# Performance work log

Hardware: AMD Instinct MI355X
Metric: run time of the kernel (lower is better)

## Reference

```python
import jax, jax.numpy as jnp
import numpy as np
from itertools import product

B = 2
X, Y, Z = 96, 96, 192          # voxel grid (x, y, t)
NPB = 300_000                   # occupied voxels per batch item
PX, PY, PZ = X // 2, Y // 2, Z // 4  # pooled grid (kernel/stride [2,2,4])
CIN, COUT, KVOL, NCONV = 32, 64, 27, 2
EPS = 1e-5


def _build_maps():
    """Builds sparse coordinates, maxpool segment ids and 3x3x3 conv kernel maps
    (gather/scatter index pairs per kernel offset), mirroring MinkowskiEngine's
    coordinate manager."""
    rng = np.random.default_rng(0)
    coords = []
    for b in range(B):
        lin = rng.choice(X * Y * Z, NPB, replace=False)
        x = lin // (Y * Z)
        y = (lin // Z) % Y
        z = lin % Z
        coords.append(np.stack([np.full(NPB, b), x, y, z], 1))
    c = np.concatenate(coords).astype(np.int64)  # [N,4] (b,x,y,z)
    # max-pool coord map: out coord = (x//2, y//2, z//4)
    pk = ((c[:, 0] * PX + c[:, 1] // 2) * PY + c[:, 2] // 2) * PZ + c[:, 3] // 4
    uniq, inv = np.unique(pk, return_inverse=True)
    M = len(uniq)
    pz = uniq % PZ
    py = (uniq // PZ) % PY
    px = (uniq // (PZ * PY)) % PX
    pb = uniq // (PZ * PY * PX)
    lut = np.full(B * PX * PY * PZ, -1, np.int64)
    lut[uniq] = np.arange(M)
    ins, outs = [], []
    for dx, dy, dz in product((-1, 0, 1), repeat=3):
        nx, ny, nz = px + dx, py + dy, pz + dz
        ok = (nx >= 0) & (nx < PX) & (ny >= 0) & (ny < PY) & (nz >= 0) & (nz < PZ)
        nk = ((pb * PX + np.clip(nx, 0, PX - 1)) * PY + np.clip(ny, 0, PY - 1)) * PZ + np.clip(nz, 0, PZ - 1)
        j = np.where(ok, lut[nk], -1)
        sel = j >= 0
        ins.append(j[sel])
        outs.append(np.arange(M)[sel])
    L = max(len(a) for a in ins)
    ci = np.full((KVOL, L), M, np.int64)  # pad -> index M (zero row)
    co = np.full((KVOL, L), M, np.int64)  # pad -> dummy out row M (dropped)
    for k in range(KVOL):
        ci[k, : len(ins[k])] = ins[k]
        co[k, : len(outs[k])] = outs[k]
    return inv.astype(np.int64), ci, co, M


def setup_inputs() -> dict:
    key = jax.random.key(0)
    ks = jax.random.split(key, 4)
    pool_seg, ci, co, M = _build_maps()
    N = B * NPB
    feats = jax.random.normal(ks[0], (N, CIN), jnp.float32)
    Wd = jax.random.normal(ks[1], (CIN, COUT), jnp.float32) / np.sqrt(CIN)
    W1 = jax.random.normal(ks[2], (KVOL, COUT, COUT), jnp.float32) / np.sqrt(KVOL * COUT)
    W2 = jax.random.normal(ks[3], (KVOL, COUT, COUT), jnp.float32) / np.sqrt(KVOL * COUT)
    ones = jnp.ones((COUT,), jnp.float32)
    zeros = jnp.zeros((COUT,), jnp.float32)
    return {
        "feats": feats, "Wd": Wd,
        "g0": ones, "b0": zeros,
        "W1": W1, "g1": ones, "b1": zeros,
        "W2": W2, "g2": ones, "b2": zeros,
        "pool_seg": jnp.asarray(pool_seg),
        "conv_in": jnp.asarray(ci), "conv_out": jnp.asarray(co),
        "num_pooled": int(M),
    }


def _bn(h, g, b):
    # training-mode batch norm over all sparse points (biased variance, eps=1e-5)
    m = h.mean(0)
    v = jnp.mean((h - m) ** 2, 0)
    return (h - m) * (g / jnp.sqrt(v + EPS)) + b


def _sparse_conv(h, W, conv_in, conv_out, M):
    # gather-GEMM-scatter over 27 kernel offsets (MinkowskiConvolution, bias=False)
    C = W.shape[-1]
    hp = jnp.concatenate([h, jnp.zeros((1, h.shape[1]), h.dtype)])  # zero pad row
    out = jnp.zeros((M + 1, C), h.dtype)
    for k in range(W.shape[0]):
        out = out.at[conv_out[k]].add(hp[conv_in[k]] @ W[k])
    return out[:M]


def reference(feats, Wd, g0, b0, W1, g1, b1, W2, g2, b2,
              pool_seg, conv_in, conv_out, num_pooled):
    # down_conv (1x1, bias=False) -> BN -> ELU
    h = jax.nn.elu(_bn(feats @ Wd, g0, b0))
    # MinkowskiMaxPooling kernel=stride=[2,2,4] == segment max over pooled cells
    down = jax.ops.segment_max(h, pool_seg, num_segments=num_pooled)
    # nConvs LUConv blocks: ELU(BN(conv3x3x3(x)))
    o = down
    for W, g, b in ((W1, g1, b1), (W2, g2, b2)):
        o = jax.nn.elu(_bn(_sparse_conv(o, W, conv_in, conv_out, num_pooled), g, b))
    # residual add + ELU
    return jax.nn.elu(o + down)
```

## Files before the change

kernel.cpp:

```cpp
#include <hip/hip_runtime.h>
#include <math.h>

#define CIN  32
#define COUT 64
#define KVOL 27
#define EPSF 1e-5f

typedef __attribute__((ext_vector_type(8))) short          short8;
typedef __attribute__((ext_vector_type(8))) unsigned short u16x8;
typedef __attribute__((ext_vector_type(4))) float          float4v;

__device__ __forceinline__ float eluf(float x) { return x > 0.f ? x : expm1f(x); }

__device__ __forceinline__ unsigned short f2bf(float x) {
    unsigned u = __float_as_uint(x);
    unsigned r = (u + 0x7FFFu + ((u >> 16) & 1u)) >> 16;
    return (unsigned short)r;
}
__device__ __forceinline__ unsigned pk2bf(float lo, float hi) {
    return (unsigned)f2bf(lo) | ((unsigned)f2bf(hi) << 16);
}
__device__ __forceinline__ float bf2f(unsigned short h) {
    return __uint_as_float(((unsigned)h) << 16);
}

__global__ void cvt_w_kernel(const float* __restrict__ W1, const float* __restrict__ W2,
                             const float* __restrict__ Wd,
                             unsigned short* __restrict__ Wt1, unsigned short* __restrict__ Wt2,
                             unsigned short* __restrict__ Wdt)
{
    int b = blockIdx.x;
    int t = threadIdx.x;
    if (b == 54) {
        for (int e = t; e < CIN * COUT; e += 256) {
            int i = e >> 6, c = e & 63;
            Wdt[c * CIN + i] = f2bf(Wd[e]);
        }
        return;
    }
    const float* W = (b < 27) ? W1 : W2;
    unsigned short* Wt = (b < 27) ? Wt1 : Wt2;
    int k = (b < 27) ? b : b - 27;
    const float* src = W + (size_t)k * (COUT * COUT);
    unsigned short* dst = Wt + (size_t)k * (COUT * COUT);
    for (int e = t; e < COUT * COUT; e += 256) {
        int i = e >> 6, c = e & 63;
        dst[c * COUT + i] = f2bf(src[e]);
    }
}

__global__ __launch_bounds__(256) void gemm_t_kernel(
    const float* __restrict__ feats, const unsigned short* __restrict__ Wdt,
    int N, unsigned short* __restrict__ t_bf, float* __restrict__ red0)
{
    __shared__ float red_s[64];
    __shared__ float red_q[64];
    int t = threadIdx.x;
    if (t < 64) { red_s[t] = 0.f; red_q[t] = 0.f; }
    __syncthreads();

    int w = t >> 6, lane = t & 63, l15 = lane & 15, quad = lane >> 4;

    short8 aw[4];
    #pragma unroll
    for (int mt = 0; mt < 4; ++mt)
        aw[mt] = *(const short8*)(Wdt + (size_t)(16 * mt + l15) * CIN + quad * 8);

    float s1[16], sq[16];
    #pragma unroll
    for (int e = 0; e < 16; ++e) { s1[e] = 0.f; sq[e] = 0.f; }

    int numTiles = (N + 15) >> 4;
    int stride = gridDim.x * 4;
    int tile = blockIdx.x * 4 + w;

    float4 c0 = make_float4(0.f, 0.f, 0.f, 0.f), c1 = c0;
    {
        int pt = tile * 16 + l15;
        if (tile < numTiles && pt < N) {
            const float4* s = (const float4*)(feats + (size_t)pt * CIN + quad * 8);
            c0 = s[0]; c1 = s[1];
        }
    }

    while (tile < numTiles) {
        int nt = tile + stride;
        float4 n0 = make_float4(0.f, 0.f, 0.f, 0.f), n1 = n0;
        {
            int npt = nt * 16 + l15;
            if (nt < numTiles && npt < N) {
                const float4* s = (const float4*)(feats + (size_t)npt * CIN + quad * 8);
                n0 = s[0]; n1 = s[1];
            }
        }
        union { short8 v; unsigned u[4]; } b;
        b.u[0] = pk2bf(c0.x, c0.y);
        b.u[1] = pk2bf(c0.z, c0.w);
        b.u[2] = pk2bf(c1.x, c1.y);
        b.u[3] = pk2bf(c1.z, c1.w);

        float4v acc[4];
        #pragma unroll
        for (int mt = 0; mt < 4; ++mt)
            acc[mt] = __builtin_amdgcn_mfma_f32_16x16x32_bf16(
                aw[mt], b.v, (float4v){0.f, 0.f, 0.f, 0.f}, 0, 0, 0);

        int pt = tile * 16 + l15;
        if (pt < N) {
            #pragma unroll
            for (int mt = 0; mt < 4; ++mt) {
                uint2 o;
                o.x = pk2bf(acc[mt][0], acc[mt][1]);
                o.y = pk2bf(acc[mt][2], acc[mt][3]);
                *(uint2*)(t_bf + (size_t)pt * COUT + mt * 16 + quad * 4) = o;
            }
        }
        #pragma unroll
        for (int mt = 0; mt < 4; ++mt)
            #pragma unroll
            for (int e = 0; e < 4; ++e) {
                float v = acc[mt][e];
                s1[mt * 4 + e] += v; sq[mt * 4 + e] += v * v;
            }
        c0 = n0; c1 = n1;
        tile = nt;
    }

    #pragma unroll
    for (int m = 1; m <= 8; m <<= 1) {
        #pragma unroll
        for (int e = 0; e < 16; ++e) {
            s1[e] += __shfl_xor(s1[e], m);
            sq[e] += __shfl_xor(sq[e], m);
        }
    }
    if (l15 == 0) {
        #pragma unroll
        for (int e = 0; e < 16; ++e) {
            int ch = (e >> 2) * 16 + quad * 4 + (e & 3);
            atomicAdd(&red_s[ch], s1[e]);
            atomicAdd(&red_q[ch], sq[e]);
        }
    }
    __syncthreads();
    float* dst = red0 + (size_t)(blockIdx.x & 3) * 128;
    if (t < 64)       atomicAdd(&dst[t], red_s[t]);
    else if (t < 128) atomicAdd(&dst[t], red_q[t - 64]);
}

__global__ void fin0_kernel(const float* __restrict__ red, const float* __restrict__ g,
                            const float* __restrict__ b, float* __restrict__ scale,
                            float* __restrict__ shift, int cnt)
{
    int c = threadIdx.x;
    float s = 0.f, q = 0.f;
    #pragma unroll
    for (int i = 0; i < 4; ++i) { s += red[i * 128 + c]; q += red[i * 128 + 64 + c]; }
    float m = s / (float)cnt;
    float var = q / (float)cnt - m * m;
    float sc = g[c] / sqrtf(var + EPSF);
    scale[c] = sc;
    shift[c] = b[c] - m * sc;
}

__global__ void bucket_kernel(const int* __restrict__ pool_seg,
                              int* __restrict__ cnt, int* __restrict__ bucket, int N)
{
    int j = blockIdx.x * 256 + threadIdx.x;
    if (j < N) {
        int s = pool_seg[j];
        int pos = atomicAdd(&cnt[s], 1);
        bucket[(size_t)s * 16 + pos] = j;
    }
}

__global__ __launch_bounds__(256) void pool_max_kernel(
    const unsigned short* __restrict__ t_bf,
    const int* __restrict__ cnt, const int* __restrict__ bucket,
    const float* __restrict__ scale0, const float* __restrict__ shift0,
    unsigned short* __restrict__ down_bf, int M)
{
    int id = blockIdx.x * 256 + threadIdx.x;
    int s = id >> 4, cg = id & 15;
    if (s >= M) return;
    int n = cnt[s];
    const int4* bk4 = (const int4*)(bucket + (size_t)s * 16);
    float4 mx = make_float4(-INFINITY, -INFINITY, -INFINITY, -INFINITY);
    float4 mn = make_float4( INFINITY,  INFINITY,  INFINITY,  INFINITY);
    #pragma unroll
    for (int ch = 0; ch < 4; ++ch) {
        if (ch * 4 >= n) break;
        int4 b4 = bk4[ch];
        #pragma unroll
        for (int e = 0; e < 4; ++e) {
            int p = ch * 4 + e;
            if (p < n) {
                int idx = (e == 0) ? b4.x : (e == 1) ? b4.y : (e == 2) ? b4.z : b4.w;
                ushort4 v = *(const ushort4*)(t_bf + (size_t)idx * COUT + cg * 4);
                float f0 = bf2f(v.x), f1 = bf2f(v.y), f2 = bf2f(v.z), f3 = bf2f(v.w);
                mx.x = fmaxf(mx.x, f0); mn.x = fminf(mn.x, f0);
                mx.y = fmaxf(mx.y, f1); mn.y = fminf(mn.y, f1);
                mx.z = fmaxf(mx.z, f2); mn.z = fminf(mn.z, f2);
                mx.w = fmaxf(mx.w, f3); mn.w = fminf(mn.w, f3);
            }
        }
    }
    int c0 = cg * 4;
    float4 sc = *(const float4*)(scale0 + c0);
    float4 sh = *(const float4*)(shift0 + c0);
    ushort4 o;
    o.x = f2bf(eluf(sc.x * (sc.x >= 0.f ? mx.x : mn.x) + sh.x));
    o.y = f2bf(eluf(sc.y * (sc.y >= 0.f ? mx.y : mn.y) + sh.y));
    o.z = f2bf(eluf(sc.z * (sc.z >= 0.f ? mx.z : mn.z) + sh.z));
    o.w = f2bf(eluf(sc.w * (sc.w >= 0.f ? mx.w : mn.w) + sh.w));
    *(ushort4*)(down_bf + (size_t)s * COUT + c0) = o;
}

__global__ void nbr_kernel(const int* __restrict__ conv_out, const int* __restrict__ conv_in,
                           int* __restrict__ nbrT, int L, int M)
{
    int k = blockIdx.y;
    int idx = blockIdx.x * 256 + threadIdx.x;
    if (idx < L) {
        int e = k * L + idx;
        int j = conv_out[e];
        if (j < M) nbrT[(size_t)k * M + j] = conv_in[e];
    }
}

__global__ void bn_elu_cvt_kernel(const float* __restrict__ o1,
                                  const float* __restrict__ scale,
                                  const float* __restrict__ shift,
                                  unsigned short* __restrict__ o1t, int n4)
{
    int i = blockIdx.x * 256 + threadIdx.x;
    if (i < n4) {
        float4 v = ((const float4*)o1)[i];
        int c0 = (i & 15) * 4;
        float4 sc = *(const float4*)(scale + c0);
        float4 sh = *(const float4*)(shift + c0);
        ushort4 o;
        o.x = f2bf(eluf(v.x * sc.x + sh.x));
        o.y = f2bf(eluf(v.y * sc.y + sh.y));
        o.z = f2bf(eluf(v.z * sc.z + sh.z));
        o.w = f2bf(eluf(v.w * sc.w + sh.w));
        ((ushort4*)o1t)[i] = o;
    }
}

__global__ __launch_bounds__(256) void conv_mfma_kernel(
    const unsigned short* __restrict__ in, const unsigned short* __restrict__ Wt,
    const int* __restrict__ nbrT, int M,
    float* __restrict__ out, float* __restrict__ red)
{
    __shared__ __align__(16) unsigned short A_lds[2][128 * 64];
    __shared__ __align__(16) unsigned short W_lds[2][64 * 64];
    __shared__ float red_s[64];
    __shared__ float red_q[64];
    int t = threadIdx.x;
    int base = blockIdx.x * 128;
    int w = t >> 6, lane = t & 63, l15 = lane & 15, quad = lane >> 4;

    if (t < 64) { red_s[t] = 0.f; red_q[t] = 0.f; }

    float4v acc[2][4];
    #pragma unroll
    for (int s = 0; s < 2; ++s)
        #pragma unroll
        for (int n = 0; n < 4; ++n)
            acc[s][n] = (float4v){0.f, 0.f, 0.f, 0.f};

    int ar = t >> 1, ah = t & 1;
    int gj = base + ar;
    int wc = t >> 2, wq = t & 3;
    int arx = ar & 7;
    int wcx = wc & 7;

    const u16x8 z8 = (u16x8){0, 0, 0, 0, 0, 0, 0, 0};

    {
        int idx0 = (gj < M) ? nbrT[gj] : -1;
        u16x8 a0 = z8, a1 = z8, a2 = z8, a3 = z8;
        if (idx0 >= 0) {
            const u16x8* src = (const u16x8*)(in + (size_t)idx0 * COUT);
            a0 = src[ah * 4 + 0]; a1 = src[ah * 4 + 1];
            a2 = src[ah * 4 + 2]; a3 = src[ah * 4 + 3];
        }
        const u16x8* ws = (const u16x8*)(Wt + (size_t)wc * COUT);
        u16x8 w0 = ws[wq * 2], w1 = ws[wq * 2 + 1];

        unsigned short* Ab = A_lds[0];
        *(u16x8*)(Ab + ar * 64 + ((ah * 4 + 0) ^ arx) * 8) = a0;
        *(u16x8*)(Ab + ar * 64 + ((ah * 4 + 1) ^ arx) * 8) = a1;
        *(u16x8*)(Ab + ar * 64 + ((ah * 4 + 2) ^ arx) * 8) = a2;
        *(u16x8*)(Ab + ar * 64 + ((ah * 4 + 3) ^ arx) * 8) = a3;
        unsigned short* Wb = W_lds[0];
        *(u16x8*)(Wb + wc * 64 + ((wq * 2 + 0) ^ wcx) * 8) = w0;
        *(u16x8*)(Wb + wc * 64 + ((wq * 2 + 1) ^ wcx) * 8) = w1;
    }
    int idxN = (gj < M) ? nbrT[(size_t)M + gj] : -1;
    __syncthreads();

    for (int k = 0; k < KVOL; ++k) {
        int cur = k & 1;
        bool pf = (k + 1 < KVOL);

        u16x8 na0 = z8, na1 = z8, na2 = z8, na3 = z8, nw0 = z8, nw1 = z8;
        if (pf) {
            if (idxN >= 0) {
                const u16x8* src = (const u16x8*)(in + (size_t)idxN * COUT);
                na0 = src[ah * 4 + 0]; na1 = src[ah * 4 + 1];
                na2 = src[ah * 4 + 2]; na3 = src[ah * 4 + 3];
            }
            const u16x8* ws = (const u16x8*)(Wt + (size_t)(k + 1) * (COUT * COUT) + (size_t)wc * COUT);
            nw0 = ws[wq * 2]; nw1 = ws[wq * 2 + 1];
            idxN = (k + 2 < KVOL && gj < M) ? nbrT[(size_t)(k + 2) * M + gj] : -1;
        }

        const unsigned short* Ab = A_lds[cur];
        const unsigned short* Wb = W_lds[cur];
        #pragma unroll
        for (int kk = 0; kk < 64; kk += 32) {
            int slb = quad + (kk >> 3);
            int r0 = 32 * w + l15;
            short8 a0 = *(const short8*)(Ab + r0 * 64 + ((slb ^ (r0 & 7)) * 8));
            int r1 = r0 + 16;
            short8 a1 = *(const short8*)(Ab + r1 * 64 + ((slb ^ (r1 & 7)) * 8));
            #pragma unroll
            for (int n = 0; n < 4; ++n) {
                int rb = 16 * n + l15;
                short8 b = *(const short8*)(Wb + rb * 64 + ((slb ^ (rb & 7)) * 8));
                acc[0][n] = __builtin_amdgcn_mfma_f32_16x16x32_bf16(a0, b, acc[0][n], 0, 0, 0);
                acc[1][n] = __builtin_amdgcn_mfma_f32_16x16x32_bf16(a1, b, acc[1][n], 0, 0, 0);
            }
        }

        if (pf) {
            unsigned short* An = A_lds[cur ^ 1];
            *(u16x8*)(An + ar * 64 + ((ah * 4 + 0) ^ arx) * 8) = na0;
            *(u16x8*)(An + ar * 64 + ((ah * 4 + 1) ^ arx) * 8) = na1;
            *(u16x8*)(An + ar * 64 + ((ah * 4 + 2) ^ arx) * 8) = na2;
            *(u16x8*)(An + ar * 64 + ((ah * 4 + 3) ^ arx) * 8) = na3;
            unsigned short* Wn = W_lds[cur ^ 1];
            *(u16x8*)(Wn + wc * 64 + ((wq * 2 + 0) ^ wcx) * 8) = nw0;
            *(u16x8*)(Wn + wc * 64 + ((wq * 2 + 1) ^ wcx) * 8) = nw1;
        }
        __syncthreads();
    }

    #pragma unroll
    for (int s = 0; s < 2; ++s) {
        int row = base + 32 * w + 16 * s + quad * 4;
        #pragma unroll
        for (int n = 0; n < 4; ++n) {
            int c = 16 * n + l15;
            #pragma unroll
            for (int e = 0; e < 4; ++e)
                if (row + e < M) out[(size_t)(row + e) * COUT + c] = acc[s][n][e];
        }
    }
    #pragma unroll
    for (int n = 0; n < 4; ++n) {
        float s1 = 0.f, sq = 0.f;
        #pragma unroll
        for (int s = 0; s < 2; ++s)
            #pragma unroll
            for (int e = 0; e < 4; ++e) { float v = acc[s][n][e]; s1 += v; sq += v * v; }
        s1 += __shfl_xor(s1, 16); sq += __shfl_xor(sq, 16);
        s1 += __shfl_xor(s1, 32); sq += __shfl_xor(sq, 32);
        if (quad == 0) {
            atomicAdd(&red_s[16 * n + l15], s1);
            atomicAdd(&red_q[16 * n + l15], sq);
        }
    }
    __syncthreads();
    if (t < 64)       atomicAdd(&red[t], red_s[t]);
    else if (t < 128) atomicAdd(&red[t], red_q[t - 64]);
}

__global__ void finC_kernel(const float* __restrict__ red, const float* __restrict__ g,
                            const float* __restrict__ b, float* __restrict__ scale,
                            float* __restrict__ shift, int M)
{
    int c = threadIdx.x;
    float m = red[c] / (float)M;
    float var = red[64 + c] / (float)M - m * m;
    float sc = g[c] / sqrtf(var + EPSF);
    scale[c] = sc;
    shift[c] = b[c] - m * sc;
}

__global__ void final_kernel(float* __restrict__ out, const unsigned short* __restrict__ down_bf,
                             const float* __restrict__ scale2, const float* __restrict__ shift2,
                             int n4)
{
    int i = blockIdx.x * 256 + threadIdx.x;
    if (i < n4) {
        float4 v = ((const float4*)out)[i];
        ushort4 d = ((const ushort4*)down_bf)[i];
        int c0 = (i & 15) * 4;
        float4 sc = *(const float4*)(scale2 + c0);
        float4 sh = *(const float4*)(shift2 + c0);
        v.x = eluf(eluf(v.x * sc.x + sh.x) + bf2f(d.x));
        v.y = eluf(eluf(v.y * sc.y + sh.y) + bf2f(d.y));
        v.z = eluf(eluf(v.z * sc.z + sh.z) + bf2f(d.z));
        v.w = eluf(eluf(v.w * sc.w + sh.w) + bf2f(d.w));
        ((float4*)out)[i] = v;
    }
}

extern "C" void kernel_launch(void* const* d_in, const int* in_sizes, int n_in,
                              void* d_out, int out_size, void* d_ws, size_t ws_size,
                              hipStream_t stream)
{
    (void)n_in; (void)ws_size;
    const float* feats    = (const float*)d_in[0];
    const float* Wd       = (const float*)d_in[1];
    const float* g0       = (const float*)d_in[2];
    const float* b0       = (const float*)d_in[3];
    const float* W1       = (const float*)d_in[4];
    const float* g1       = (const float*)d_in[5];
    const float* b1       = (const float*)d_in[6];
    const float* W2       = (const float*)d_in[7];
    const float* g2       = (const float*)d_in[8];
    const float* b2       = (const float*)d_in[9];
    const int*   pool_seg = (const int*)d_in[10];
    const int*   conv_in  = (const int*)d_in[11];
    const int*   conv_out = (const int*)d_in[12];

    int N = in_sizes[0] / CIN;
    int M = out_size / COUT;
    int L = in_sizes[11] / KVOL;

    char* ws = (char*)d_ws;
    size_t off = 0;
    auto alloc = [&](size_t bytes) -> void* {
        void* p = ws + off;
        off = (off + bytes + 255) & ~(size_t)255;
        return p;
    };
    float*          o1      = (float*)alloc((size_t)M * COUT * 4);
    unsigned short* down_bf = (unsigned short*)alloc((size_t)M * COUT * 2);
    unsigned short* o1t     = (unsigned short*)alloc((size_t)M * COUT * 2);
    unsigned short* t_bf    = (unsigned short*)alloc((size_t)N * COUT * 2);
    int*            nbrT    = (int*)alloc((size_t)KVOL * M * 4);
    unsigned short* Wt1     = (unsigned short*)alloc((size_t)KVOL * COUT * COUT * 2);
    unsigned short* Wt2     = (unsigned short*)alloc((size_t)KVOL * COUT * COUT * 2);
    unsigned short* Wdt     = (unsigned short*)alloc((size_t)CIN * COUT * 2);
    int*            cnt     = (int*)alloc((size_t)M * 4);
    int*            bucket  = (int*)alloc((size_t)M * 16 * 4);
    float* red  = (float*)alloc((size_t)768 * 4);
    float* red0 = red, *red1 = red + 512, *red2 = red + 640;
    float* sreg = (float*)alloc((size_t)6 * 64 * 4);
    float* scale0 = sreg, *shift0 = sreg + 64;
    float* scale1 = sreg + 128, *shift1 = sreg + 192;
    float* scale2 = sreg + 256, *shift2 = sreg + 320;

    hipMemsetAsync(nbrT, 0xFF, (size_t)KVOL * M * 4, stream);
    hipMemsetAsync(cnt, 0, (size_t)M * 4, stream);
    hipMemsetAsync(red, 0, (size_t)768 * 4, stream);

    cvt_w_kernel<<<55, 256, 0, stream>>>(W1, W2, Wd, Wt1, Wt2, Wdt);
    gemm_t_kernel<<<1024, 256, 0, stream>>>(feats, Wdt, N, t_bf, red0);
    fin0_kernel<<<1, 64, 0, stream>>>(red0, g0, b0, scale0, shift0, N);
    bucket_kernel<<<(N + 255) / 256, 256, 0, stream>>>(pool_seg, cnt, bucket, N);
    pool_max_kernel<<<(M * 16 + 255) / 256, 256, 0, stream>>>(
        t_bf, cnt, bucket, scale0, shift0, down_bf, M);
    dim3 gn((L + 255) / 256, KVOL);
    nbr_kernel<<<gn, 256, 0, stream>>>(conv_out, conv_in, nbrT, L, M);

    int cblocks = (M + 127) / 128;
    conv_mfma_kernel<<<cblocks, 256, 0, stream>>>(down_bf, Wt1, nbrT, M, o1, red1);
    finC_kernel<<<1, 64, 0, stream>>>(red1, g1, b1, scale1, shift1, M);
    int n4 = (M * COUT) / 4;
    bn_elu_cvt_kernel<<<(n4 + 255) / 256, 256, 0, stream>>>(o1, scale1, shift1, o1t, n4);
    conv_mfma_kernel<<<cblocks, 256, 0, stream>>>(o1t, Wt2, nbrT, M, (float*)d_out, red2);
    finC_kernel<<<1, 64, 0, stream>>>(red2, g2, b2, scale2, shift2, M);
    final_kernel<<<(n4 + 255) / 256, 256, 0, stream>>>(
        (float*)d_out, down_bf, scale2, shift2, n4);
}
```

Measured before the change: 529.4 us.

## Double conv tile to 256 rows with 512 threads and XCD-aware block remap

```diff
diff --git a/kernel.cpp b/kernel.cpp
--- a/kernel.cpp
+++ b/kernel.cpp
@@ -248,20 +248,22 @@
     }
 }
 
-__global__ __launch_bounds__(256) void conv_mfma_kernel(
+__global__ __launch_bounds__(512) void conv_mfma_kernel(
     const unsigned short* __restrict__ in, const unsigned short* __restrict__ Wt,
     const int* __restrict__ nbrT, int M,
     float* __restrict__ out, float* __restrict__ red)
 {
-    __shared__ __align__(16) unsigned short A_lds[2][128 * 64];
+    __shared__ __align__(16) unsigned short A_lds[2][256 * 64];
     __shared__ __align__(16) unsigned short W_lds[2][64 * 64];
-    __shared__ float red_s[64];
-    __shared__ float red_q[64];
     int t = threadIdx.x;
-    int base = blockIdx.x * 128;
+
+    int nwg = gridDim.x;
+    int q = nwg >> 3, r = nwg & 7;
+    int xcd = blockIdx.x & 7, pos = blockIdx.x >> 3;
+    int sb = (xcd < r ? xcd * (q + 1) : r * (q + 1) + (xcd - r) * q) + pos;
+    int base = sb * 256;
+
     int w = t >> 6, lane = t & 63, l15 = lane & 15, quad = lane >> 4;
-
-    if (t < 64) { red_s[t] = 0.f; red_q[t] = 0.f; }
 
     float4v acc[2][4];
     #pragma unroll
@@ -272,8 +274,8 @@
 
     int ar = t >> 1, ah = t & 1;
     int gj = base + ar;
-    int wc = t >> 2, wq = t & 3;
     int arx = ar & 7;
+    int wc = t >> 3, wq = t & 7;
     int wcx = wc & 7;
 
     const u16x8 z8 = (u16x8){0, 0, 0, 0, 0, 0, 0, 0};
@@ -282,21 +284,17 @@
         int idx0 = (gj < M) ? nbrT[gj] : -1;
         u16x8 a0 = z8, a1 = z8, a2 = z8, a3 = z8;
         if (idx0 >= 0) {
-            const u16x8* src = (const u16x8*)(in + (size_t)idx0 * COUT);
-            a0 = src[ah * 4 + 0]; a1 = src[ah * 4 + 1];
-            a2 = src[ah * 4 + 2]; a3 = src[ah * 4 + 3];
-        }
-        const u16x8* ws = (const u16x8*)(Wt + (size_t)wc * COUT);
-        u16x8 w0 = ws[wq * 2], w1 = ws[wq * 2 + 1];
+            const u16x8* src = (const u16x8*)(in + (size_t)idx0 * COUT + 32 * ah);
+            a0 = src[0]; a1 = src[1]; a2 = src[2]; a3 = src[3];
+        }
+        u16x8 w0 = *(const u16x8*)(Wt + (size_t)wc * COUT + wq * 8);
 
         unsigned short* Ab = A_lds[0];
         *(u16x8*)(Ab + ar * 64 + ((ah * 4 + 0) ^ arx) * 8) = a0;
         *(u16x8*)(Ab + ar * 64 + ((ah * 4 + 1) ^ arx) * 8) = a1;
         *(u16x8*)(Ab + ar * 64 + ((ah * 4 + 2) ^ arx) * 8) = a2;
         *(u16x8*)(Ab + ar * 64 + ((ah * 4 + 3) ^ arx) * 8) = a3;
-        unsigned short* Wb = W_lds[0];
-        *(u16x8*)(Wb + wc * 64 + ((wq * 2 + 0) ^ wcx) * 8) = w0;
-        *(u16x8*)(Wb + wc * 64 + ((wq * 2 + 1) ^ wcx) * 8) = w1;
+        *(u16x8*)(W_lds[0] + wc * 64 + ((wq ^ wcx) * 8)) = w0;
     }
     int idxN = (gj < M) ? nbrT[(size_t)M + gj] : -1;
     __syncthreads();
@@ -305,15 +303,13 @@
         int cur = k & 1;
         bool pf = (k + 1 < KVOL);
 
-        u16x8 na0 = z8, na1 = z8, na2 = z8, na3 = z8, nw0 = z8, nw1 = z8;
+        u16x8 na0 = z8, na1 = z8, na2 = z8, na3 = z8, nw0 = z8;
         if (pf) {
             if (idxN >= 0) {
-                const u16x8* src = (const u16x8*)(in + (size_t)idxN * COUT);
-                na0 = src[ah * 4 + 0]; na1 = src[ah * 4 + 1];
-                na2 = src[ah * 4 + 2]; na3 = src[ah * 4 + 3];
-            }
-            const u16x8* ws = (const u16x8*)(Wt + (size_t)(k + 1) * (COUT * COUT) + (size_t)wc * COUT);
-            nw0 = ws[wq * 2]; nw1 = ws[wq * 2 + 1];
+                const u16x8* src = (const u16x8*)(in + (size_t)idxN * COUT + 32 * ah);
+                na0 = src[0]; na1 = src[1]; na2 = src[2]; na3 = src[3];
+            }
+            nw0 = *(const u16x8*)(Wt + (size_t)(k + 1) * (COUT * COUT) + (size_t)wc * COUT + wq * 8);
             idxN = (k + 2 < KVOL && gj < M) ? nbrT[(size_t)(k + 2) * M + gj] : -1;
         }
 
@@ -341,9 +337,7 @@
             *(u16x8*)(An + ar * 64 + ((ah * 4 + 1) ^ arx) * 8) = na1;
             *(u16x8*)(An + ar * 64 + ((ah * 4 + 2) ^ arx) * 8) = na2;
             *(u16x8*)(An + ar * 64 + ((ah * 4 + 3) ^ arx) * 8) = na3;
-            unsigned short* Wn = W_lds[cur ^ 1];
-            *(u16x8*)(Wn + wc * 64 + ((wq * 2 + 0) ^ wcx) * 8) = nw0;
-            *(u16x8*)(Wn + wc * 64 + ((wq * 2 + 1) ^ wcx) * 8) = nw1;
+            *(u16x8*)(W_lds[cur ^ 1] + wc * 64 + ((wq ^ wcx) * 8)) = nw0;
         }
         __syncthreads();
     }
@@ -359,6 +353,11 @@
                 if (row + e < M) out[(size_t)(row + e) * COUT + c] = acc[s][n][e];
         }
     }
+
+    float* red_s = (float*)(W_lds[0]);
+    float* red_q = red_s + 64;
+    if (t < 128) red_s[t] = 0.f;
+    __syncthreads();
     #pragma unroll
     for (int n = 0; n < 4; ++n) {
         float s1 = 0.f, sq = 0.f;
@@ -469,12 +468,12 @@
     dim3 gn((L + 255) / 256, KVOL);
     nbr_kernel<<<gn, 256, 0, stream>>>(conv_out, conv_in, nbrT, L, M);
 
-    int cblocks = (M + 127) / 128;
-    conv_mfma_kernel<<<cblocks, 256, 0, stream>>>(down_bf, Wt1, nbrT, M, o1, red1);
+    int cblocks = (M + 255) / 256;
+    conv_mfma_kernel<<<cblocks, 512, 0, stream>>>(down_bf, Wt1, nbrT, M, o1, red1);
     finC_kernel<<<1, 64, 0, stream>>>(red1, g1, b1, scale1, shift1, M);
     int n4 = (M * COUT) / 4;
     bn_elu_cvt_kernel<<<(n4 + 255) / 256, 256, 0, stream>>>(o1, scale1, shift1, o1t, n4);
-    conv_mfma_kernel<<<cblocks, 256, 0, stream>>>(o1t, Wt2, nbrT, M, (float*)d_out, red2);
+    conv_mfma_kernel<<<cblocks, 512, 0, stream>>>(o1t, Wt2, nbrT, M, (float*)d_out, red2);
     finC_kernel<<<1, 64, 0, stream>>>(red2, g2, b2, scale2, shift2, M);
     final_kernel<<<(n4 + 255) / 256, 256, 0, stream>>>(
         (float*)d_out, down_bf, scale2, shift2, n4);
```

New measurement: 491.3 us. -7.2%, faster.
